# Kernel tuning notes

Hardware: AMD Instinct MI355X
Metric: run time of the kernel (lower is better)

## Reference

```python
import jax, jax.numpy as jnp
import numpy as np

D_MODEL = 1024
N_HEAD = 16
HEAD_SIZE = D_MODEL // N_HEAD


def setup_inputs() -> dict:
    key = jax.random.key(0)
    ks = jax.random.split(key, 7)
    B, T, E = 2, 2048, D_MODEL
    scale = 0.02
    return {
        "q": jax.random.normal(ks[0], (B, T, E), dtype=jnp.float32),
        "k": jax.random.normal(ks[1], (B, T, E), dtype=jnp.float32),
        "v": jax.random.normal(ks[2], (B, T, E), dtype=jnp.float32),
        "Wq": jax.random.normal(ks[3], (E, E), dtype=jnp.float32) * scale,
        "Wk": jax.random.normal(ks[4], (E, E), dtype=jnp.float32) * scale,
        "Wv": jax.random.normal(ks[5], (E, E), dtype=jnp.float32) * scale,
        "Wo": jax.random.normal(ks[6], (E, E), dtype=jnp.float32) * scale,
    }


def reference(q, k, v, Wq, Wk, Wv, Wo):
    B, T, E = q.shape
    # torch nn.Linear(bias=False): y = x @ W.T
    qh = (q @ Wq.T).reshape(B, T, N_HEAD, HEAD_SIZE).transpose(0, 2, 1, 3)  # [B,H,T,Dh]
    kh = (k @ Wk.T).reshape(B, T, N_HEAD, HEAD_SIZE).transpose(0, 2, 1, 3)
    vh = (v @ Wv.T).reshape(B, T, N_HEAD, HEAD_SIZE).transpose(0, 2, 1, 3)

    scale = 1.0 / jnp.sqrt(jnp.asarray(HEAD_SIZE, dtype=q.dtype))
    wei = jnp.einsum("bhqd,bhkd->bhqk", qh, kh) * scale  # [B,H,T,T]

    # causal mask (tril): positions j > i set to -inf
    causal = jnp.tril(jnp.ones((T, T), dtype=bool))
    wei = jnp.where(causal, wei, jnp.asarray(-jnp.inf, dtype=wei.dtype))

    attn = jax.nn.softmax(wei, axis=-1)
    out = jnp.einsum("bhqk,bhkd->bhqd", attn, vh)  # [B,H,T,Dh]
    out = out.transpose(0, 2, 1, 3).reshape(B, T, E)
    return out @ Wo.T  # dropout p=0.0 -> identity
```

## Files before the change

kernel.cpp:

```cpp
#include <hip/hip_runtime.h>
#include <hip/hip_bf16.h>
#include <cstddef>
#include <cstdint>

#define B_SZ   2
#define T_SEQ  2048
#define E_DIM  1024
#define N_HEAD 16
#define HEAD   64

typedef unsigned short u16;
using frag8 = __attribute__((ext_vector_type(8))) short;
using f32x4 = __attribute__((ext_vector_type(4))) float;

__device__ inline u16 f2bf(float x) {
    __hip_bfloat16 h = __float2bfloat16(x);
    return *reinterpret_cast<u16*>(&h);
}

__device__ inline void gl2lds16(const void* g, void* l) {
    auto gp = reinterpret_cast<const __attribute__((address_space(1))) unsigned int*>(
        reinterpret_cast<uintptr_t>(g));
    auto lp = reinterpret_cast<__attribute__((address_space(3))) unsigned int*>(
        reinterpret_cast<uintptr_t>(l));
    __builtin_amdgcn_global_load_lds(gp, lp, 16, 0, 0);
}

struct CastArgs {
    const float* src[7];
    u16* dst[7];
    int n[7];
    float scale[7];
};

__global__ __launch_bounds__(256) void cast_f32_bf16(CastArgs a) {
    const int t = blockIdx.y;
    const int i0 = (blockIdx.x * 256 + threadIdx.x) * 8;
    if (i0 >= a.n[t]) return;
    const float sc = a.scale[t];
    const float4 f0 = *(const float4*)(a.src[t] + i0);
    const float4 f1 = *(const float4*)(a.src[t] + i0 + 4);
    union { u16 s[8]; uint4 v; } r;
    r.s[0] = f2bf(f0.x * sc); r.s[1] = f2bf(f0.y * sc);
    r.s[2] = f2bf(f0.z * sc); r.s[3] = f2bf(f0.w * sc);
    r.s[4] = f2bf(f1.x * sc); r.s[5] = f2bf(f1.y * sc);
    r.s[6] = f2bf(f1.z * sc); r.s[7] = f2bf(f1.w * sc);
    *(uint4*)(a.dst[t] + i0) = r.v;
}

__device__ inline void gemm_core(const u16* __restrict__ X,
                                 const u16* __restrict__ W,
                                 void* __restrict__ Yv, int mode,
                                 int bm0, int bn0) {
    __shared__ u16 As[64 * 64];
    __shared__ u16 Bs[128 * 64];

    const int tid = threadIdx.x;
    const int w = tid >> 6;
    const int lane = tid & 63;
    const int ln = lane & 15;
    const int quad = lane >> 4;
    const int wm = (w & 1) * 32;
    const int wn = (w >> 1) * 64;

    const int l8 = lane >> 3;
    const int g = (lane & 7) ^ l8;

    const u16* Ag = X + (size_t)(bm0 + w * 16 + l8) * 1024 + g * 8;
    const u16* Bg = W + (size_t)(bn0 + w * 32 + l8) * 1024 + g * 8;
    const int al = __builtin_amdgcn_readfirstlane(w * 1024);
    const int bl = __builtin_amdgcn_readfirstlane(w * 2048);

    const f32x4 zf = {0.f, 0.f, 0.f, 0.f};
    f32x4 acc[2][4];
#pragma unroll
    for (int mi = 0; mi < 2; ++mi)
#pragma unroll
        for (int nj = 0; nj < 4; ++nj) acc[mi][nj] = zf;

    const int sw = ln & 7;

    for (int k0 = 0; k0 < 1024; k0 += 64) {
        gl2lds16(Ag + k0, As + al);
        gl2lds16(Ag + 8 * 1024 + k0, As + al + 512);
#pragma unroll
        for (int i = 0; i < 4; ++i)
            gl2lds16(Bg + i * 8 * 1024 + k0, Bs + bl + i * 512);
        __syncthreads();

        frag8 a[2][2], b[4][2];
#pragma unroll
        for (int kc = 0; kc < 2; ++kc) {
            const int slot = ((kc * 4 + quad) ^ sw) * 8;
#pragma unroll
            for (int mi = 0; mi < 2; ++mi)
                a[mi][kc] = *(const frag8*)(As + (wm + mi * 16 + ln) * 64 + slot);
#pragma unroll
            for (int nj = 0; nj < 4; ++nj)
                b[nj][kc] = *(const frag8*)(Bs + (wn + nj * 16 + ln) * 64 + slot);
        }
#pragma unroll
        for (int kc = 0; kc < 2; ++kc)
#pragma unroll
            for (int mi = 0; mi < 2; ++mi)
#pragma unroll
                for (int nj = 0; nj < 4; ++nj)
                    acc[mi][nj] = __builtin_amdgcn_mfma_f32_16x16x32_bf16(
                        a[mi][kc], b[nj][kc], acc[mi][nj], 0, 0, 0);
        __syncthreads();
    }

#pragma unroll
    for (int mi = 0; mi < 2; ++mi)
#pragma unroll
        for (int nj = 0; nj < 4; ++nj)
#pragma unroll
            for (int reg = 0; reg < 4; ++reg) {
                const int m = bm0 + wm + mi * 16 + quad * 4 + reg;
                const int n = bn0 + wn + nj * 16 + ln;
                if (mode == 1) {
                    ((float*)Yv)[(size_t)m * E_DIM + n] = acc[mi][nj][reg];
                } else {
                    const int b_ = m >> 11, t_ = m & (T_SEQ - 1);
                    const int h_ = n >> 6, d_ = n & (HEAD - 1);
                    const size_t idx = (mode == 0)
                        ? (((size_t)(b_ * N_HEAD + h_)) * T_SEQ + t_) * HEAD + d_
                        : (((size_t)(b_ * N_HEAD + h_)) * HEAD + d_) * T_SEQ + t_;
                    ((u16*)Yv)[idx] = f2bf(acc[mi][nj][reg]);
                }
            }
}

struct QkvArgs {
    const u16* X[3];
    const u16* W[3];
    u16* Y[3];
};

__global__ __launch_bounds__(256) void gemm_qkv(QkvArgs a) {
    const int z = blockIdx.z;
    gemm_core(a.X[z], a.W[z], a.Y[z], z == 2 ? 2 : 0,
              blockIdx.x * 64, blockIdx.y * 128);
}

__global__ __launch_bounds__(256) void gemm_out(const u16* __restrict__ X,
                                                const u16* __restrict__ W,
                                                float* __restrict__ Y) {
    gemm_core(X, W, Y, 1, blockIdx.x * 64, blockIdx.y * 128);
}

__global__ __launch_bounds__(256) void attn_mfma(const u16* __restrict__ Qh,
                                                 const u16* __restrict__ Kh,
                                                 const u16* __restrict__ Vt_g,
                                                 u16* __restrict__ Aa) {
    __shared__ u16 Ks[128][72];
    __shared__ u16 Vs[64][136];
    __shared__ u16 Ps[4][32][136];

    const int tid = threadIdx.x;
    const int w = tid >> 6;
    const int lane = tid & 63;
    const int ln = lane & 15;
    const int quad = lane >> 4;

    const int i = blockIdx.x;
    const int half = i >> 8;
    const int r_ = i & 255;
    const int bh = r_ >> 3;
    const int j = r_ & 7;
    const int qt = half ? j : (15 - j);
    const int q0 = qt * 128;
    const int qw = q0 + w * 32;

    const size_t base = (size_t)bh * T_SEQ * HEAD;
    const u16* Qb = Qh + base;
    const u16* Kb = Kh + base;
    const u16* Vtb = Vt_g + base;

    frag8 qf[2][2];
#pragma unroll
    for (int mi = 0; mi < 2; ++mi)
#pragma unroll
        for (int kc = 0; kc < 2; ++kc)
            qf[mi][kc] = *(const frag8*)(Qb + (size_t)(qw + mi * 16 + ln) * HEAD +
                                         kc * 32 + quad * 8);

    const f32x4 zf = {0.f, 0.f, 0.f, 0.f};
    f32x4 o[2][4];
    float rsl[2][4];
#pragma unroll
    for (int mi = 0; mi < 2; ++mi) {
#pragma unroll
        for (int nj = 0; nj < 4; ++nj) o[mi][nj] = zf;
#pragma unroll
        for (int reg = 0; reg < 4; ++reg) rsl[mi][reg] = 0.f;
    }

    for (int kt = 0; kt <= qt; ++kt) {
        const int k0 = kt << 7;
        const bool diag = (kt == qt);
        __syncthreads();
#pragma unroll
        for (int it = 0; it < 4; ++it) {
            const int idx = tid + it * 256;
            const int kr = idx >> 3, kc_ = idx & 7;
            *(uint4*)&Ks[kr][kc_ * 8] =
                *(const uint4*)(Kb + (size_t)(k0 + kr) * HEAD + kc_ * 8);
            const int vr = idx >> 4, vc = idx & 15;
            *(uint4*)&Vs[vr][vc * 8] =
                *(const uint4*)(Vtb + (size_t)vr * T_SEQ + k0 + vc * 8);
        }
        __syncthreads();

        f32x4 s[2][8];
#pragma unroll
        for (int mi = 0; mi < 2; ++mi)
#pragma unroll
            for (int nj = 0; nj < 8; ++nj) s[mi][nj] = zf;
#pragma unroll
        for (int kc = 0; kc < 2; ++kc)
#pragma unroll
            for (int nj = 0; nj < 8; ++nj) {
                const frag8 bk = *(const frag8*)&Ks[nj * 16 + ln][kc * 32 + quad * 8];
#pragma unroll
                for (int mi = 0; mi < 2; ++mi)
                    s[mi][nj] = __builtin_amdgcn_mfma_f32_16x16x32_bf16(
                        qf[mi][kc], bk, s[mi][nj], 0, 0, 0);
            }

#pragma unroll
        for (int mi = 0; mi < 2; ++mi)
#pragma unroll
            for (int nj = 0; nj < 8; ++nj)
#pragma unroll
                for (int reg = 0; reg < 4; ++reg) {
                    float e = __expf(s[mi][nj][reg]);
                    if (diag) {
                        const int key = k0 + nj * 16 + ln;
                        const int qr = qw + mi * 16 + quad * 4 + reg;
                        e = (key <= qr) ? e : 0.f;
                    }
                    rsl[mi][reg] += e;
                    Ps[w][mi * 16 + quad * 4 + reg][nj * 16 + ln] = f2bf(e);
                }

#pragma unroll
        for (int kc = 0; kc < 4; ++kc) {
            frag8 pa[2];
#pragma unroll
            for (int mi = 0; mi < 2; ++mi)
                pa[mi] = *(const frag8*)&Ps[w][mi * 16 + ln][kc * 32 + quad * 8];
#pragma unroll
            for (int nj = 0; nj < 4; ++nj) {
                const frag8 bv = *(const frag8*)&Vs[nj * 16 + ln][kc * 32 + quad * 8];
#pragma unroll
                for (int mi = 0; mi < 2; ++mi)
                    o[mi][nj] = __builtin_amdgcn_mfma_f32_16x16x32_bf16(
                        pa[mi], bv, o[mi][nj], 0, 0, 0);
            }
        }
    }

#pragma unroll
    for (int msk = 1; msk < 16; msk <<= 1)
#pragma unroll
        for (int mi = 0; mi < 2; ++mi)
#pragma unroll
            for (int reg = 0; reg < 4; ++reg)
                rsl[mi][reg] += __shfl_xor(rsl[mi][reg], msk, 16);

    const int b_ = bh >> 4, h_ = bh & (N_HEAD - 1);
#pragma unroll
    for (int mi = 0; mi < 2; ++mi) {
        float inv[4];
#pragma unroll
        for (int reg = 0; reg < 4; ++reg) inv[reg] = 1.f / rsl[mi][reg];
#pragma unroll
        for (int nj = 0; nj < 4; ++nj)
#pragma unroll
            for (int reg = 0; reg < 4; ++reg) {
                const int q = qw + mi * 16 + quad * 4 + reg;
                const int d = nj * 16 + ln;
                Aa[((size_t)(b_ * T_SEQ + q)) * E_DIM + h_ * HEAD + d] =
                    f2bf(o[mi][nj][reg] * inv[reg]);
            }
    }
}

extern "C" void kernel_launch(void* const* d_in, const int* in_sizes, int n_in,
                              void* d_out, int out_size, void* d_ws, size_t ws_size,
                              hipStream_t stream) {
    const float* q  = (const float*)d_in[0];
    const float* k  = (const float*)d_in[1];
    const float* v  = (const float*)d_in[2];
    const float* Wq = (const float*)d_in[3];
    const float* Wk = (const float*)d_in[4];
    const float* Wv = (const float*)d_in[5];
    const float* Wo = (const float*)d_in[6];

    u16* ws = (u16*)d_ws;
    const size_t M4 = (size_t)4 * 1024 * 1024;
    const size_t M1 = (size_t)1024 * 1024;
    u16* qb  = ws;
    u16* kb  = ws + M4;
    u16* vb  = ws + 2 * M4;
    u16* Wqb = ws + 3 * M4;
    u16* Wkb = ws + 3 * M4 + M1;
    u16* Wvb = ws + 3 * M4 + 2 * M1;
    u16* Wob = ws + 3 * M4 + 3 * M1;
    u16* Qh  = ws + 4 * M4;
    u16* Kh  = ws + 5 * M4;
    u16* Vht = ws + 6 * M4;
    u16* Aa  = ws + 7 * M4;

    CastArgs ca;
    ca.src[0] = q;  ca.src[1] = k;  ca.src[2] = v;
    ca.src[3] = Wq; ca.src[4] = Wk; ca.src[5] = Wv; ca.src[6] = Wo;
    ca.dst[0] = qb;  ca.dst[1] = kb;  ca.dst[2] = vb;
    ca.dst[3] = Wqb; ca.dst[4] = Wkb; ca.dst[5] = Wvb; ca.dst[6] = Wob;
    ca.n[0] = ca.n[1] = ca.n[2] = (int)M4;
    ca.n[3] = ca.n[4] = ca.n[5] = ca.n[6] = (int)M1;
    ca.scale[0] = ca.scale[1] = ca.scale[2] = 1.f;
    ca.scale[3] = 0.125f;
    ca.scale[4] = ca.scale[5] = ca.scale[6] = 1.f;
    cast_f32_bf16<<<dim3(2048, 7), 256, 0, stream>>>(ca);

    QkvArgs ga;
    ga.X[0] = qb;  ga.X[1] = kb;  ga.X[2] = vb;
    ga.W[0] = Wqb; ga.W[1] = Wkb; ga.W[2] = Wvb;
    ga.Y[0] = Qh;  ga.Y[1] = Kh;  ga.Y[2] = Vht;
    gemm_qkv<<<dim3(64, 8, 3), 256, 0, stream>>>(ga);

    attn_mfma<<<dim3(512), 256, 0, stream>>>(Qh, Kh, Vht, Aa);

    gemm_out<<<dim3(64, 8), 256, 0, stream>>>(Aa, Wob, (float*)d_out);
}
```

Baseline: 244.9 us.

## Restructure attention kernel with double-buffered async LDS loads and register-resident P

```diff
diff --git a/kernel.cpp b/kernel.cpp
--- a/kernel.cpp
+++ b/kernel.cpp
@@ -10,6 +10,7 @@
 #define HEAD   64
 
 typedef unsigned short u16;
+typedef unsigned int u32;
 using frag8 = __attribute__((ext_vector_type(8))) short;
 using f32x4 = __attribute__((ext_vector_type(4))) float;
 
@@ -149,13 +150,12 @@
     gemm_core(X, W, Y, 1, blockIdx.x * 64, blockIdx.y * 128);
 }
 
-__global__ __launch_bounds__(256) void attn_mfma(const u16* __restrict__ Qh,
-                                                 const u16* __restrict__ Kh,
-                                                 const u16* __restrict__ Vt_g,
-                                                 u16* __restrict__ Aa) {
-    __shared__ u16 Ks[128][72];
-    __shared__ u16 Vs[64][136];
-    __shared__ u16 Ps[4][32][136];
+__global__ __launch_bounds__(256, 4) void attn_mfma(const u16* __restrict__ Qh,
+                                                    const u16* __restrict__ Kh,
+                                                    const u16* __restrict__ Vt_g,
+                                                    u16* __restrict__ Aa) {
+    __shared__ u16 Ks[2][64 * 64];
+    __shared__ u16 Vs[2][64 * 64];
 
     const int tid = threadIdx.x;
     const int w = tid >> 6;
@@ -177,112 +177,153 @@
     const u16* Kb = Kh + base;
     const u16* Vtb = Vt_g + base;
 
+    const int l8 = lane >> 3;
+    const int g = (lane & 7) ^ l8;
+    const int kls = __builtin_amdgcn_readfirstlane(w * 16 * 64);
+    const int vls = __builtin_amdgcn_readfirstlane(w * 16 * 64);
+
     frag8 qf[2][2];
 #pragma unroll
-    for (int mi = 0; mi < 2; ++mi)
+    for (int qq = 0; qq < 2; ++qq)
 #pragma unroll
         for (int kc = 0; kc < 2; ++kc)
-            qf[mi][kc] = *(const frag8*)(Qb + (size_t)(qw + mi * 16 + ln) * HEAD +
+            qf[qq][kc] = *(const frag8*)(Qb + (size_t)(qw + qq * 16 + ln) * HEAD +
                                          kc * 32 + quad * 8);
 
     const f32x4 zf = {0.f, 0.f, 0.f, 0.f};
-    f32x4 o[2][4];
-    float rsl[2][4];
-#pragma unroll
-    for (int mi = 0; mi < 2; ++mi) {
-#pragma unroll
-        for (int nj = 0; nj < 4; ++nj) o[mi][nj] = zf;
-#pragma unroll
-        for (int reg = 0; reg < 4; ++reg) rsl[mi][reg] = 0.f;
-    }
-
-    for (int kt = 0; kt <= qt; ++kt) {
-        const int k0 = kt << 7;
-        const bool diag = (kt == qt);
+    f32x4 o[4][2];
+    float rsl[2] = {0.f, 0.f};
+#pragma unroll
+    for (int dt = 0; dt < 4; ++dt)
+#pragma unroll
+        for (int qq = 0; qq < 2; ++qq) o[dt][qq] = zf;
+
+    const int ktiles = 2 * qt + 2;
+
+    {
+        const int k0 = 0;
+#pragma unroll
+        for (int it = 0; it < 2; ++it) {
+            const int rb = w * 16 + it * 8;
+            gl2lds16(Kb + (size_t)(k0 + rb + l8) * HEAD + g * 8,
+                     &Ks[0][0] + kls + it * 512);
+            gl2lds16(Vtb + (size_t)(rb + l8) * T_SEQ + k0 + g * 8,
+                     &Vs[0][0] + vls + it * 512);
+        }
+    }
+
+    const int sw = ln & 7;
+
+    for (int kt = 0; kt < ktiles; ++kt) {
+        const int k0 = kt * 64;
+        const int buf = kt & 1;
         __syncthreads();
-#pragma unroll
-        for (int it = 0; it < 4; ++it) {
-            const int idx = tid + it * 256;
-            const int kr = idx >> 3, kc_ = idx & 7;
-            *(uint4*)&Ks[kr][kc_ * 8] =
-                *(const uint4*)(Kb + (size_t)(k0 + kr) * HEAD + kc_ * 8);
-            const int vr = idx >> 4, vc = idx & 15;
-            *(uint4*)&Vs[vr][vc * 8] =
-                *(const uint4*)(Vtb + (size_t)vr * T_SEQ + k0 + vc * 8);
+
+        if (kt + 1 < ktiles) {
+            const int k1 = k0 + 64;
+#pragma unroll
+            for (int it = 0; it < 2; ++it) {
+                const int rb = w * 16 + it * 8;
+                gl2lds16(Kb + (size_t)(k1 + rb + l8) * HEAD + g * 8,
+                         &Ks[buf ^ 1][0] + kls + it * 512);
+                gl2lds16(Vtb + (size_t)(rb + l8) * T_SEQ + k1 + g * 8,
+                         &Vs[buf ^ 1][0] + vls + it * 512);
+            }
         }
-        __syncthreads();
-
-        f32x4 s[2][8];
-#pragma unroll
-        for (int mi = 0; mi < 2; ++mi)
-#pragma unroll
-            for (int nj = 0; nj < 8; ++nj) s[mi][nj] = zf;
-#pragma unroll
-        for (int kc = 0; kc < 2; ++kc)
-#pragma unroll
-            for (int nj = 0; nj < 8; ++nj) {
-                const frag8 bk = *(const frag8*)&Ks[nj * 16 + ln][kc * 32 + quad * 8];
-#pragma unroll
-                for (int mi = 0; mi < 2; ++mi)
-                    s[mi][nj] = __builtin_amdgcn_mfma_f32_16x16x32_bf16(
-                        qf[mi][kc], bk, s[mi][nj], 0, 0, 0);
-            }
-
-#pragma unroll
-        for (int mi = 0; mi < 2; ++mi)
-#pragma unroll
-            for (int nj = 0; nj < 8; ++nj)
-#pragma unroll
-                for (int reg = 0; reg < 4; ++reg) {
-                    float e = __expf(s[mi][nj][reg]);
-                    if (diag) {
-                        const int key = k0 + nj * 16 + ln;
-                        const int qr = qw + mi * 16 + quad * 4 + reg;
-                        e = (key <= qr) ? e : 0.f;
+
+        if (k0 <= qw + 31) {
+            f32x4 st[4][2];
+#pragma unroll
+            for (int kk = 0; kk < 4; ++kk)
+#pragma unroll
+                for (int qq = 0; qq < 2; ++qq) st[kk][qq] = zf;
+#pragma unroll
+            for (int kc = 0; kc < 2; ++kc) {
+                const int slot = ((kc * 4 + quad) ^ sw) * 8;
+#pragma unroll
+                for (int kk = 0; kk < 4; ++kk) {
+                    const frag8 kf = *(const frag8*)(&Ks[buf][0] + (kk * 16 + ln) * 64 + slot);
+#pragma unroll
+                    for (int qq = 0; qq < 2; ++qq)
+                        st[kk][qq] = __builtin_amdgcn_mfma_f32_16x16x32_bf16(
+                            kf, qf[qq][kc], st[kk][qq], 0, 0, 0);
+                }
+            }
+
+            const bool msk = (k0 + 63 > qw);
+            u32 pk[4][2][2];
+#pragma unroll
+            for (int kk = 0; kk < 4; ++kk)
+#pragma unroll
+                for (int qq = 0; qq < 2; ++qq) {
+                    float e[4];
+#pragma unroll
+                    for (int reg = 0; reg < 4; ++reg) {
+                        const int key = k0 + kk * 16 + quad * 4 + reg;
+                        const int qg = qw + qq * 16 + ln;
+                        float ev = __expf(st[kk][qq][reg]);
+                        if (msk) ev = (key <= qg) ? ev : 0.f;
+                        e[reg] = ev;
+                        rsl[qq] += ev;
                     }
-                    rsl[mi][reg] += e;
-                    Ps[w][mi * 16 + quad * 4 + reg][nj * 16 + ln] = f2bf(e);
-                }
-
-#pragma unroll
-        for (int kc = 0; kc < 4; ++kc) {
-            frag8 pa[2];
-#pragma unroll
-            for (int mi = 0; mi < 2; ++mi)
-                pa[mi] = *(const frag8*)&Ps[w][mi * 16 + ln][kc * 32 + quad * 8];
-#pragma unroll
-            for (int nj = 0; nj < 4; ++nj) {
-                const frag8 bv = *(const frag8*)&Vs[nj * 16 + ln][kc * 32 + quad * 8];
-#pragma unroll
-                for (int mi = 0; mi < 2; ++mi)
-                    o[mi][nj] = __builtin_amdgcn_mfma_f32_16x16x32_bf16(
-                        pa[mi], bv, o[mi][nj], 0, 0, 0);
+                    pk[kk][qq][0] = ((u32)f2bf(e[1]) << 16) | f2bf(e[0]);
+                    pk[kk][qq][1] = ((u32)f2bf(e[3]) << 16) | f2bf(e[2]);
+                }
+
+            const int hsel = quad >> 1;
+            const int s_lo = ((quad & 1) * 2) * 16 + ln;
+            const int s_hi = s_lo + 16;
+#pragma unroll
+            for (int kc = 0; kc < 2; ++kc) {
+                union { frag8 f; u32 d[4]; } pb[2];
+#pragma unroll
+                for (int qq = 0; qq < 2; ++qq) {
+                    const u32 a00 = __shfl(pk[kc * 2][qq][0], s_lo, 64);
+                    const u32 a01 = __shfl(pk[kc * 2][qq][1], s_lo, 64);
+                    const u32 a02 = __shfl(pk[kc * 2][qq][0], s_hi, 64);
+                    const u32 a03 = __shfl(pk[kc * 2][qq][1], s_hi, 64);
+                    const u32 a10 = __shfl(pk[kc * 2 + 1][qq][0], s_lo, 64);
+                    const u32 a11 = __shfl(pk[kc * 2 + 1][qq][1], s_lo, 64);
+                    const u32 a12 = __shfl(pk[kc * 2 + 1][qq][0], s_hi, 64);
+                    const u32 a13 = __shfl(pk[kc * 2 + 1][qq][1], s_hi, 64);
+                    pb[qq].d[0] = hsel ? a10 : a00;
+                    pb[qq].d[1] = hsel ? a11 : a01;
+                    pb[qq].d[2] = hsel ? a12 : a02;
+                    pb[qq].d[3] = hsel ? a13 : a03;
+                }
+                const int slot = ((kc * 4 + quad) ^ sw) * 8;
+#pragma unroll
+                for (int dt = 0; dt < 4; ++dt) {
+                    const frag8 vf = *(const frag8*)(&Vs[buf][0] + (dt * 16 + ln) * 64 + slot);
+#pragma unroll
+                    for (int qq = 0; qq < 2; ++qq)
+                        o[dt][qq] = __builtin_amdgcn_mfma_f32_16x16x32_bf16(
+                            vf, pb[qq].f, o[dt][qq], 0, 0, 0);
+                }
             }
         }
     }
 
 #pragma unroll
-    for (int msk = 1; msk < 16; msk <<= 1)
-#pragma unroll
-        for (int mi = 0; mi < 2; ++mi)
-#pragma unroll
-            for (int reg = 0; reg < 4; ++reg)
-                rsl[mi][reg] += __shfl_xor(rsl[mi][reg], msk, 16);
-
+    for (int qq = 0; qq < 2; ++qq) {
+        rsl[qq] += __shfl_xor(rsl[qq], 16, 64);
+        rsl[qq] += __shfl_xor(rsl[qq], 32, 64);
+    }
+    const float inv0 = 1.f / rsl[0];
+    const float inv1 = 1.f / rsl[1];
     const int b_ = bh >> 4, h_ = bh & (N_HEAD - 1);
 #pragma unroll
-    for (int mi = 0; mi < 2; ++mi) {
-        float inv[4];
-#pragma unroll
-        for (int reg = 0; reg < 4; ++reg) inv[reg] = 1.f / rsl[mi][reg];
-#pragma unroll
-        for (int nj = 0; nj < 4; ++nj)
-#pragma unroll
-            for (int reg = 0; reg < 4; ++reg) {
-                const int q = qw + mi * 16 + quad * 4 + reg;
-                const int d = nj * 16 + ln;
-                Aa[((size_t)(b_ * T_SEQ + q)) * E_DIM + h_ * HEAD + d] =
-                    f2bf(o[mi][nj][reg] * inv[reg]);
+    for (int qq = 0; qq < 2; ++qq) {
+        const float inv = qq ? inv1 : inv0;
+        const int qg = qw + qq * 16 + ln;
+        u16* rowp = Aa + ((size_t)(b_ * T_SEQ + qg)) * E_DIM + h_ * HEAD;
+#pragma unroll
+        for (int dt = 0; dt < 4; ++dt)
+#pragma unroll
+            for (int rp = 0; rp < 2; ++rp) {
+                const u32 v = ((u32)f2bf(o[dt][qq][2 * rp + 1] * inv) << 16) |
+                              f2bf(o[dt][qq][2 * rp] * inv);
+                *(u32*)(rowp + dt * 16 + quad * 4 + rp * 2) = v;
             }
     }
 }
```

After: 220.3 us. 10.1% less time.
